# Performance work log

Measured on AMD Instinct MI355X. Metric: run time of the kernel, lower is better.

The kernel has to match this reference:

```python
import jax, jax.numpy as jnp
import numpy as np

B, T, N, D, H, NMASK = 8192, 2, 40, 64, 1, 3
EPS = 1e-5


def setup_inputs() -> dict:
    key = jax.random.key(0)
    ks = jax.random.split(key, 12)
    F = T * N * 2 * D  # flattened feature size fed to BatchNorm1d
    return {
        "x": jax.random.normal(ks[0], (B, N, D), jnp.float32),
        "masker": jax.random.uniform(ks[1], (T, NMASK, N, N), jnp.float32, -0.27, 0.27),  # xavier-like
        "ln_gamma": jnp.ones((N,), jnp.float32),
        "ln_beta": jnp.zeros((N,), jnp.float32),
        "gnn_w": jax.random.normal(ks[2], (1, T, H, 2 * D, D), jnp.float32) * 0.05,
        "gnn_b": jax.random.normal(ks[3], (T, H, N, D), jnp.float32) * 0.05,
        "bn_gamma": jnp.ones((H, F), jnp.float32),
        "bn_beta": jnp.zeros((H, F), jnp.float32),
        "bn_mean": jax.random.normal(ks[4], (H, F), jnp.float32) * 0.1,
        "bn_var": jax.random.uniform(ks[5], (H, F), jnp.float32, 0.5, 1.5),
        "gate_w": jax.random.normal(ks[6], (N * D, N), jnp.float32) * 0.02,
        "gate_b": jnp.zeros((N,), jnp.float32),
    }


def reference(x, masker, ln_gamma, ln_beta, gnn_w, gnn_b, bn_gamma, bn_beta, bn_mean, bn_var, gate_w, gate_b):
    b = x.shape[0]
    # broadcast input to towers: (B, T, N, D)
    h = jnp.broadcast_to(x[:, None], (b, T, N, D))
    # adjacency from product of mask matrices: (T, N, N)
    adj = jax.nn.relu(jnp.prod(masker, axis=1))
    mask = (adj != 0).astype(x.dtype)
    # LayerNorm(num_fields) applied on transposed adj == normalize over rows (axis -2)
    mu = adj.mean(axis=-2, keepdims=True)
    var = adj.var(axis=-2, keepdims=True)
    ln = (adj - mu) / jnp.sqrt(var + EPS) * ln_gamma[:, None] + ln_beta[:, None]
    x_masked = ln + (1.0 - mask) * (-1e9) + jnp.eye(N, dtype=x.dtype)
    # softmax over rows (dim=1 of (T,N,N)) then re-mask
    A = jax.nn.softmax(x_masked, axis=1) * mask  # (T, N, N)
    for idx in range(H):
        # nei[b,t,n,d] = sum_m h[b,t,m,d] * A[t,m,n]
        nei = jnp.einsum('btmd,tmn->btnd', h, A)
        hc = jnp.concatenate([h, nei], axis=-1)  # (B,T,N,2D)
        flat = hc.reshape(b, -1)
        flat = (flat - bn_mean[idx]) / jnp.sqrt(bn_var[idx] + EPS) * bn_gamma[idx] + bn_beta[idx]
        hc = flat.reshape(b, T, N, 2 * D)
        # per-tower transform: (B,T,N,2D) x (T,2D,D) -> (B,T,N,D)
        h = jnp.einsum('btnf,tfd->btnd', hc, gnn_w[0, :, idx]) + gnn_b[:, idx]
    # attention pooling over fields
    logits = h.reshape(b, T, N * D) @ gate_w + gate_b  # (B,T,N)
    w = jax.nn.softmax(logits, axis=2)
    return jnp.sum(h * w[..., None], axis=2)  # (B, T, D)
```

## Files before the change

### kernel.cpp

```cpp
#include <hip/hip_runtime.h>
#include <hip/hip_bf16.h>
#include <stdint.h>

typedef float v4f __attribute__((ext_vector_type(4)));
typedef short v8s __attribute__((ext_vector_type(8)));

#define NB 40

__device__ __forceinline__ unsigned short f2b(float f) {
  __hip_bfloat16 h = __float2bfloat16(f);
  unsigned short u;
  __builtin_memcpy(&u, &h, 2);
  return u;
}
__device__ __forceinline__ unsigned pk2(float lo, float hi) {
  __hip_bfloat162 h = __float22bfloat162_rn(make_float2(lo, hi));
  unsigned u;
  __builtin_memcpy(&u, &h, 4);
  return u;
}
__device__ __forceinline__ float b2f16(unsigned short h) {
  return __uint_as_float(((unsigned)h) << 16);
}
__device__ __forceinline__ float blo(unsigned u) { return __uint_as_float(u << 16); }
__device__ __forceinline__ float bhi(unsigned u) { return __uint_as_float(u & 0xFFFF0000u); }


__global__ __launch_bounds__(256) void prep(
    const float* __restrict__ x, const float* __restrict__ masker,
    const float* __restrict__ ln_gamma, const float* __restrict__ ln_beta,
    const float* __restrict__ gnn_w, const float* __restrict__ gnn_b,
    const float* __restrict__ bn_gamma, const float* __restrict__ bn_beta,
    const float* __restrict__ bn_mean, const float* __restrict__ bn_var,
    const float* __restrict__ gate_w,
    unsigned short* __restrict__ A1pk, unsigned short* __restrict__ W2pk,
    unsigned short* __restrict__ Gpk, float* __restrict__ s1,
    float* __restrict__ sNT, float* __restrict__ bias2T,
    unsigned short* __restrict__ xk, unsigned short* __restrict__ xb16)
{
  __shared__ float AtL[2 * NB * NB];
  const int tid = threadIdx.x;

  {
    const int lane = tid & 63, bq = tid >> 6;
    const int b = blockIdx.x * 4 + bq;
    const float* xb = x + (size_t)b * 2560 + lane;
    unsigned u[20];
    #pragma unroll
    for (int mp = 0; mp < 20; ++mp)
      u[mp] = pk2(xb[(2*mp)*64], xb[(2*mp+1)*64]);
    unsigned short* dst = xk + ((size_t)b * 64 + lane) * 40;
    #pragma unroll
    for (int i = 0; i < 5; ++i)
      *(uint4*)(dst + i*8) = make_uint4(u[4*i], u[4*i+1], u[4*i+2], u[4*i+3]);
    const float4* xs4 = (const float4*)(x + (size_t)blockIdx.x * 10240);
    uint2* xd2 = (uint2*)(xb16 + (size_t)blockIdx.x * 10240);
    #pragma unroll
    for (int it = 0; it < 10; ++it) {
      float4 v = xs4[it*256 + tid];
      xd2[it*256 + tid] = make_uint2(pk2(v.x, v.y), pk2(v.z, v.w));
    }
  }

  if (blockIdx.x < 40) {
    const int gid = blockIdx.x * 256 + tid, gsz = 40 * 256;
    for (int e = gid; e < 16384; e += gsz) {
      int frag = e >> 9, rem = e & 511, lane = rem >> 3, jj = rem & 7;
      int t = frag >> 4, ks = (frag >> 2) & 3, dt = frag & 3;
      int f = ks*32 + (lane >> 4)*8 + jj, d = dt*16 + (lane & 15);
      W2pk[e] = f2b(gnn_w[t*8192 + f*64 + d]);
    }
    for (int e = gid; e < 122880; e += gsz) {
      int frag = e >> 9, rem = e & 511, lane = rem >> 3, jj = rem & 7;
      int kt = frag / 3, jt = frag % 3;
      int fl = kt*32 + (lane >> 4)*8 + jj, j = jt*16 + (lane & 15);
      Gpk[e] = f2b(j < NB ? gate_w[fl*NB + j] : 0.f);
    }
    for (int e = gid; e < 5120; e += gsz) {
      int t = e / 2560, n = (e % 2560) / 64, d = e & 63;
      int F = (t*NB + n)*128 + d;
      s1[e] = bn_gamma[F] * rsqrtf(bn_var[F] + 1e-5f);
    }
    for (int e = gid; e < 5120; e += gsz) {
      int t = e / 2560, d = (e % 2560) / 40, n = e % 40;
      int F = (t*NB + n)*128 + 64 + d;
      sNT[e] = bn_gamma[F] * rsqrtf(bn_var[F] + 1e-5f);
    }
    for (int e = gid; e < 5120; e += gsz) {
      int t = e / 2560, d = (e % 2560) / 40, n = e % 40;
      float acc = gnn_b[(t*NB + n)*64 + d];
      int Fb = (t*NB + n)*128;
      for (int f = 0; f < 128; ++f) {
        float s = bn_gamma[Fb+f] * rsqrtf(bn_var[Fb+f] + 1e-5f);
        float o = bn_beta[Fb+f] - bn_mean[Fb+f] * s;
        acc += o * gnn_w[t*8192 + f*64 + d];
      }
      bias2T[e] = acc;
    }
  } else if (blockIdx.x == 40) {
    for (int col = tid; col < 2 * NB; col += 256) {
      int t = col / NB, n = col % NB;
      float adj[NB];
      for (int m = 0; m < NB; ++m) {
        float p = masker[((t*3+0)*NB+m)*NB+n]
                * masker[((t*3+1)*NB+m)*NB+n]
                * masker[((t*3+2)*NB+m)*NB+n];
        adj[m] = p > 0.f ? p : 0.f;
      }
      float mu = 0.f;
      for (int m = 0; m < NB; ++m) mu += adj[m];
      mu *= (1.f/NB);
      float var = 0.f;
      for (int m = 0; m < NB; ++m) { float dv = adj[m]-mu; var += dv*dv; }
      var *= (1.f/NB);
      float inv = rsqrtf(var + 1e-5f);
      float xm[NB]; float mx = -3e38f;
      for (int m = 0; m < NB; ++m) {
        float lnv = (adj[m]-mu)*inv*ln_gamma[m] + ln_beta[m];
        float v = lnv + (adj[m] != 0.f ? 0.f : -1e9f) + (m==n ? 1.f : 0.f);
        xm[m] = v; mx = fmaxf(mx, v);
      }
      float ssum = 0.f;
      for (int m = 0; m < NB; ++m) { xm[m] = __expf(xm[m]-mx); ssum += xm[m]; }
      float isum = 1.f/ssum;
      for (int m = 0; m < NB; ++m)
        AtL[(t*NB+n)*NB+m] = (adj[m] != 0.f) ? xm[m]*isum : 0.f;
    }
    __syncthreads();
    for (int e = tid; e < 6144; e += 256) {
      int frag = e >> 9, rem = e & 511, lane = rem >> 3, jj = rem & 7;
      int t = frag / 6, r2 = frag % 6, nt = r2 >> 1, ks = r2 & 1;
      int n = nt*16 + (lane & 15);
      int m = ks*32 + (lane >> 4)*8 + jj;
      A1pk[e] = f2b((n < NB && m < NB) ? AtL[(t*NB+n)*NB+m] : 0.f);
    }
  }
}

__global__ __launch_bounds__(256) void kernelM(
    const unsigned short* __restrict__ xb16, const unsigned short* __restrict__ xk,
    const unsigned short* __restrict__ A1pk, const unsigned short* __restrict__ W2pk,
    const unsigned short* __restrict__ Gpk, const float* __restrict__ s1,
    const float* __restrict__ sNT, const float* __restrict__ bias2T,
    const float* __restrict__ gate_b, float* __restrict__ out)
{
  __shared__ __align__(16) unsigned short hc[160 * 136];
  __shared__ __align__(16) unsigned short hL[4 * 2568];
  __shared__ float pj[16 * 48];
  __shared__ float wgt[4 * NB];

  const int tid = threadIdx.x;
  const int lane = tid & 63;
  const int w = tid >> 6;
  const int l = lane & 15, q = lane >> 4;
  const int b0 = blockIdx.x * 4;
  unsigned* hcU = (unsigned*)hc;

  v8s b1[4][2];
  #pragma unroll
  for (int i = 0; i < 4; ++i)
    #pragma unroll
    for (int ks = 0; ks < 2; ++ks)
      b1[i][ks] = *(const v8s*)(xk + ((size_t)b0*64 + (w*4+i)*16 + l)*40 + ks*32 + q*8);
  v8s a1[2][3][2];
  #pragma unroll
  for (int t = 0; t < 2; ++t)
    #pragma unroll
    for (int nt = 0; nt < 3; ++nt)
      #pragma unroll
      for (int ks = 0; ks < 2; ++ks)
        a1[t][nt][ks] = *(const v8s*)(A1pk + (((t*3+nt)*2+ks) << 9) + lane*8);
  v8s w2[2][4];
  #pragma unroll
  for (int t = 0; t < 2; ++t)
    #pragma unroll
    for (int ks = 0; ks < 4; ++ks)
      w2[t][ks] = *(const v8s*)(W2pk + (((t*4+ks)*4 + w) << 9) + lane*8);

  uint4 xr[5];

  #pragma unroll
  for (int t = 0; t < 2; ++t) {
    #pragma unroll
    for (int it = 0; it < 5; ++it) {
      const int c = it*256 + tid;
      const int row = c >> 3, dp8 = c & 7;
      if (t == 0)
        xr[it] = *(const uint4*)((const unsigned*)xb16 + (size_t)b0*1280 + row*32 + dp8*4);
      const uint4 xv = xr[it];
      const int n = row % NB;
      const float4 sA = *(const float4*)(s1 + (t*NB + n)*64 + dp8*8);
      const float4 sB = *(const float4*)(s1 + (t*NB + n)*64 + dp8*8 + 4);
      uint4 p;
      p.x = pk2(blo(xv.x)*sA.x, bhi(xv.x)*sA.y);
      p.y = pk2(blo(xv.y)*sA.z, bhi(xv.y)*sA.w);
      p.z = pk2(blo(xv.z)*sB.x, bhi(xv.z)*sB.y);
      p.w = pk2(blo(xv.w)*sB.z, bhi(xv.w)*sB.w);
      *(uint4*)(hcU + row*68 + dp8*4) = p;
    }
    #pragma unroll
    for (int i = 0; i < 4; ++i) {
      const int R = (w*4+i)*16 + l;
      const int bb = R >> 6, d = R & 63;
      #pragma unroll
      for (int nt = 0; nt < 3; ++nt) {
        v4f acc = {0.f, 0.f, 0.f, 0.f};
        acc = __builtin_amdgcn_mfma_f32_16x16x32_bf16(a1[t][nt][0], b1[i][0], acc, 0, 0, 0);
        acc = __builtin_amdgcn_mfma_f32_16x16x32_bf16(a1[t][nt][1], b1[i][1], acc, 0, 0, 0);
        const float4 sv = *(const float4*)(sNT + (t*64+d)*40 + nt*16 + q*4);
        #pragma unroll
        for (int r = 0; r < 4; ++r) {
          int n = nt*16 + q*4 + r;
          if (n < NB) hc[(bb*NB + n)*136 + 64 + d] = f2b(acc[r]*sv[r]);
        }
      }
    }
    __syncthreads();
    #pragma unroll
    for (int mt = 0; mt < 10; ++mt) {
      v4f acc = {0.f, 0.f, 0.f, 0.f};
      #pragma unroll
      for (int ks = 0; ks < 4; ++ks) {
        v8s af = *(const v8s*)(hc + (mt*16 + l)*136 + ks*32 + q*8);
        acc = __builtin_amdgcn_mfma_f32_16x16x32_bf16(af, w2[t][ks], acc, 0, 0, 0);
      }
      const int d = w*16 + l;
      const int G = mt*16 + q*4;
      const int bb = G / NB, n0 = G - bb*NB;
      const float4 bv = *(const float4*)(bias2T + (t*64+d)*40 + n0);
      #pragma unroll
      for (int r = 0; r < 4; ++r)
        hL[bb*2568 + (n0+r)*64 + d] = f2b(acc[r] + bv[r]);
    }
    __syncthreads();
    v4f ac0 = {0,0,0,0}, ac1 = {0,0,0,0}, ac2 = {0,0,0,0};
    for (int kt = w; kt < 80; kt += 4) {
      v8s bf = *(const v8s*)(hL + (l & 3)*2568 + kt*32 + q*8);
      v8s g0 = *(const v8s*)(Gpk + ((kt*3+0) << 9) + lane*8);
      v8s g1 = *(const v8s*)(Gpk + ((kt*3+1) << 9) + lane*8);
      v8s g2 = *(const v8s*)(Gpk + ((kt*3+2) << 9) + lane*8);
      ac0 = __builtin_amdgcn_mfma_f32_16x16x32_bf16(g0, bf, ac0, 0, 0, 0);
      ac1 = __builtin_amdgcn_mfma_f32_16x16x32_bf16(g1, bf, ac1, 0, 0, 0);
      ac2 = __builtin_amdgcn_mfma_f32_16x16x32_bf16(g2, bf, ac2, 0, 0, 0);
    }
    if (l < 4) {
      #pragma unroll
      for (int r = 0; r < 4; ++r) {
        pj[(w*4 + l)*48 +  0 + q*4 + r] = ac0[r];
        pj[(w*4 + l)*48 + 16 + q*4 + r] = ac1[r];
        pj[(w*4 + l)*48 + 32 + q*4 + r] = ac2[r];
      }
    }
    __syncthreads();
    if (tid < 32) {
      const int bb = tid >> 3, s = tid & 7;
      float lv[5]; float mx = -3e38f;
      #pragma unroll
      for (int i = 0; i < 5; ++i) {
        int j = s*5 + i;
        float v = gate_b[j];
        #pragma unroll
        for (int ww = 0; ww < 4; ++ww) v += pj[(ww*4 + bb)*48 + j];
        lv[i] = v; mx = fmaxf(mx, v);
      }
      #pragma unroll
      for (int m = 1; m < 8; m <<= 1) mx = fmaxf(mx, __shfl_xor(mx, m));
      float es = 0.f;
      #pragma unroll
      for (int i = 0; i < 5; ++i) { lv[i] = __expf(lv[i] - mx); es += lv[i]; }
      #pragma unroll
      for (int m = 1; m < 8; m <<= 1) es += __shfl_xor(es, m);
      float inv = 1.f / es;
      #pragma unroll
      for (int i = 0; i < 5; ++i) wgt[bb*NB + s*5 + i] = lv[i]*inv;
    }
    __syncthreads();
    {
      float accp = 0.f;
      #pragma unroll 8
      for (int n = 0; n < NB; ++n)
        accp += b2f16(hL[w*2568 + n*64 + lane]) * wgt[w*NB + n];
      out[((size_t)(b0 + w)*2 + t)*64 + lane] = accp;
    }
  }
}

extern "C" void kernel_launch(void* const* d_in, const int* in_sizes, int n_in,
                              void* d_out, int out_size, void* d_ws, size_t ws_size,
                              hipStream_t stream) {
  const float* x        = (const float*)d_in[0];
  const float* masker   = (const float*)d_in[1];
  const float* ln_gamma = (const float*)d_in[2];
  const float* ln_beta  = (const float*)d_in[3];
  const float* gnn_w    = (const float*)d_in[4];
  const float* gnn_b    = (const float*)d_in[5];
  const float* bn_gamma = (const float*)d_in[6];
  const float* bn_beta  = (const float*)d_in[7];
  const float* bn_mean  = (const float*)d_in[8];
  const float* bn_var   = (const float*)d_in[9];
  const float* gate_w   = (const float*)d_in[10];
  const float* gate_b   = (const float*)d_in[11];
  float* out = (float*)d_out;

  char* ws = (char*)d_ws;
  unsigned short* A1pk   = (unsigned short*)(ws + 0);
  unsigned short* W2pk   = (unsigned short*)(ws + 12288);
  unsigned short* Gpk    = (unsigned short*)(ws + 45056);
  float*          s1     = (float*)(ws + 290816);
  float*          sNT    = (float*)(ws + 311296);
  float*          bias2T = (float*)(ws + 331904);
  unsigned short* xk     = (unsigned short*)(ws + 352384);
  unsigned short* xb16   = (unsigned short*)(ws + 42295552);

  prep<<<2048, 256, 0, stream>>>(x, masker, ln_gamma, ln_beta, gnn_w, gnn_b,
                                 bn_gamma, bn_beta, bn_mean, bn_var, gate_w,
                                 A1pk, W2pk, Gpk, s1, sNT, bias2T, xk, xb16);
  kernelM<<<2048, 256, 0, stream>>>(xb16, xk, A1pk, W2pk, Gpk,
                                    s1, sNT, bias2T, gate_b, out);
}
```

Before: 265.1 us.

## Fuse fp32-to-bf16 input conversion into main kernel and shrink prep kernel

The prep kernel no longer converts x into two bf16 copies (xk transposed and xb16) in global memory. kernelM now reads fp32 x directly, packs it to bf16 in registers, and builds the transposed operand through shared memory. This removes a full extra write and read pass over the activations, which was the dominant memory traffic. The change also aliases hL onto hc to cut LDS use, sets launch bounds to 3 blocks per CU, loads A and W fragments per tower to reduce register pressure, splits the bias reduction across four lanes, and does the gate softmax with wave shuffles instead of a shared buffer and an extra barrier. The cost is more barriers and an LDS transpose inside the main kernel.

```diff
diff --git a/kernel.cpp b/kernel.cpp
--- a/kernel.cpp
+++ b/kernel.cpp
@@ -27,7 +27,7 @@
 
 
 __global__ __launch_bounds__(256) void prep(
-    const float* __restrict__ x, const float* __restrict__ masker,
+    const float* __restrict__ masker,
     const float* __restrict__ ln_gamma, const float* __restrict__ ln_beta,
     const float* __restrict__ gnn_w, const float* __restrict__ gnn_b,
     const float* __restrict__ bn_gamma, const float* __restrict__ bn_beta,
@@ -35,69 +35,11 @@
     const float* __restrict__ gate_w,
     unsigned short* __restrict__ A1pk, unsigned short* __restrict__ W2pk,
     unsigned short* __restrict__ Gpk, float* __restrict__ s1,
-    float* __restrict__ sNT, float* __restrict__ bias2T,
-    unsigned short* __restrict__ xk, unsigned short* __restrict__ xb16)
+    float* __restrict__ sNT, float* __restrict__ bias2T)
 {
-  __shared__ float AtL[2 * NB * NB];
   const int tid = threadIdx.x;
-
-  {
-    const int lane = tid & 63, bq = tid >> 6;
-    const int b = blockIdx.x * 4 + bq;
-    const float* xb = x + (size_t)b * 2560 + lane;
-    unsigned u[20];
-    #pragma unroll
-    for (int mp = 0; mp < 20; ++mp)
-      u[mp] = pk2(xb[(2*mp)*64], xb[(2*mp+1)*64]);
-    unsigned short* dst = xk + ((size_t)b * 64 + lane) * 40;
-    #pragma unroll
-    for (int i = 0; i < 5; ++i)
-      *(uint4*)(dst + i*8) = make_uint4(u[4*i], u[4*i+1], u[4*i+2], u[4*i+3]);
-    const float4* xs4 = (const float4*)(x + (size_t)blockIdx.x * 10240);
-    uint2* xd2 = (uint2*)(xb16 + (size_t)blockIdx.x * 10240);
-    #pragma unroll
-    for (int it = 0; it < 10; ++it) {
-      float4 v = xs4[it*256 + tid];
-      xd2[it*256 + tid] = make_uint2(pk2(v.x, v.y), pk2(v.z, v.w));
-    }
-  }
-
-  if (blockIdx.x < 40) {
-    const int gid = blockIdx.x * 256 + tid, gsz = 40 * 256;
-    for (int e = gid; e < 16384; e += gsz) {
-      int frag = e >> 9, rem = e & 511, lane = rem >> 3, jj = rem & 7;
-      int t = frag >> 4, ks = (frag >> 2) & 3, dt = frag & 3;
-      int f = ks*32 + (lane >> 4)*8 + jj, d = dt*16 + (lane & 15);
-      W2pk[e] = f2b(gnn_w[t*8192 + f*64 + d]);
-    }
-    for (int e = gid; e < 122880; e += gsz) {
-      int frag = e >> 9, rem = e & 511, lane = rem >> 3, jj = rem & 7;
-      int kt = frag / 3, jt = frag % 3;
-      int fl = kt*32 + (lane >> 4)*8 + jj, j = jt*16 + (lane & 15);
-      Gpk[e] = f2b(j < NB ? gate_w[fl*NB + j] : 0.f);
-    }
-    for (int e = gid; e < 5120; e += gsz) {
-      int t = e / 2560, n = (e % 2560) / 64, d = e & 63;
-      int F = (t*NB + n)*128 + d;
-      s1[e] = bn_gamma[F] * rsqrtf(bn_var[F] + 1e-5f);
-    }
-    for (int e = gid; e < 5120; e += gsz) {
-      int t = e / 2560, d = (e % 2560) / 40, n = e % 40;
-      int F = (t*NB + n)*128 + 64 + d;
-      sNT[e] = bn_gamma[F] * rsqrtf(bn_var[F] + 1e-5f);
-    }
-    for (int e = gid; e < 5120; e += gsz) {
-      int t = e / 2560, d = (e % 2560) / 40, n = e % 40;
-      float acc = gnn_b[(t*NB + n)*64 + d];
-      int Fb = (t*NB + n)*128;
-      for (int f = 0; f < 128; ++f) {
-        float s = bn_gamma[Fb+f] * rsqrtf(bn_var[Fb+f] + 1e-5f);
-        float o = bn_beta[Fb+f] - bn_mean[Fb+f] * s;
-        acc += o * gnn_w[t*8192 + f*64 + d];
-      }
-      bias2T[e] = acc;
-    }
-  } else if (blockIdx.x == 40) {
+  if (blockIdx.x == 0) {
+    __shared__ float AtL[2 * NB * NB];
     for (int col = tid; col < 2 * NB; col += 256) {
       int t = col / NB, n = col % NB;
       float adj[NB];
@@ -134,20 +76,57 @@
       int m = ks*32 + (lane >> 4)*8 + jj;
       A1pk[e] = f2b((n < NB && m < NB) ? AtL[(t*NB+n)*NB+m] : 0.f);
     }
+  } else {
+    const int gid = (blockIdx.x - 1) * 256 + tid, gsz = 63 * 256;
+    for (int e = gid; e < 16384; e += gsz) {
+      int frag = e >> 9, rem = e & 511, lane = rem >> 3, jj = rem & 7;
+      int t = frag >> 4, ks = (frag >> 2) & 3, dt = frag & 3;
+      int f = ks*32 + (lane >> 4)*8 + jj, d = dt*16 + (lane & 15);
+      W2pk[e] = f2b(gnn_w[t*8192 + f*64 + d]);
+    }
+    for (int e = gid; e < 122880; e += gsz) {
+      int frag = e >> 9, rem = e & 511, lane = rem >> 3, jj = rem & 7;
+      int kt = frag / 3, jt = frag % 3;
+      int fl = kt*32 + (lane >> 4)*8 + jj, j = jt*16 + (lane & 15);
+      Gpk[e] = f2b(j < NB ? gate_w[fl*NB + j] : 0.f);
+    }
+    for (int e = gid; e < 5120; e += gsz) {
+      int t = e / 2560, n = (e % 2560) / 64, d = e & 63;
+      int F = (t*NB + n)*128 + d;
+      s1[e] = bn_gamma[F] * rsqrtf(bn_var[F] + 1e-5f);
+    }
+    for (int e = gid; e < 5120; e += gsz) {
+      int t = e / 2560, d = (e % 2560) / 40, n = e % 40;
+      int F = (t*NB + n)*128 + 64 + d;
+      sNT[e] = bn_gamma[F] * rsqrtf(bn_var[F] + 1e-5f);
+    }
+    for (int e4 = gid; e4 < 20480; e4 += gsz) {
+      int e = e4 >> 2, part = e4 & 3;
+      int t = e / 2560, d = (e % 2560) / 40, n = e % 40;
+      float acc = (part == 0) ? gnn_b[(t*NB + n)*64 + d] : 0.f;
+      int Fb = (t*NB + n)*128;
+      int f0 = part * 32;
+      for (int f = f0; f < f0 + 32; ++f) {
+        float s = bn_gamma[Fb+f] * rsqrtf(bn_var[Fb+f] + 1e-5f);
+        float o = bn_beta[Fb+f] - bn_mean[Fb+f] * s;
+        acc += o * gnn_w[t*8192 + f*64 + d];
+      }
+      acc += __shfl_xor(acc, 1);
+      acc += __shfl_xor(acc, 2);
+      if (part == 0) bias2T[e] = acc;
+    }
   }
 }
 
-__global__ __launch_bounds__(256) void kernelM(
-    const unsigned short* __restrict__ xb16, const unsigned short* __restrict__ xk,
+__global__ __launch_bounds__(256, 3) void kernelM(
+    const float* __restrict__ x,
     const unsigned short* __restrict__ A1pk, const unsigned short* __restrict__ W2pk,
     const unsigned short* __restrict__ Gpk, const float* __restrict__ s1,
     const float* __restrict__ sNT, const float* __restrict__ bias2T,
     const float* __restrict__ gate_b, float* __restrict__ out)
 {
   __shared__ __align__(16) unsigned short hc[160 * 136];
-  __shared__ __align__(16) unsigned short hL[4 * 2568];
   __shared__ float pj[16 * 48];
-  __shared__ float wgt[4 * NB];
 
   const int tid = threadIdx.x;
   const int lane = tid & 63;
@@ -155,38 +134,61 @@
   const int l = lane & 15, q = lane >> 4;
   const int b0 = blockIdx.x * 4;
   unsigned* hcU = (unsigned*)hc;
-
+  unsigned short* hL = hc;
+
+  uint4 xr[5];
+  #pragma unroll
+  for (int it = 0; it < 5; ++it) {
+    const int c = it * 256 + tid, row = c >> 3, dp8 = c & 7;
+    const float* xp = x + (size_t)b0 * 2560 + row * 64 + dp8 * 8;
+    const float4 f0 = *(const float4*)xp;
+    const float4 f1 = *(const float4*)(xp + 4);
+    xr[it] = make_uint4(pk2(f0.x, f0.y), pk2(f0.z, f0.w),
+                        pk2(f1.x, f1.y), pk2(f1.z, f1.w));
+  }
+  if (tid < 12) hcU[5120 + tid] = 0u;
+  #pragma unroll
+  for (int it = 0; it < 5; ++it) {
+    const int c = it * 256 + tid, row = c >> 3, dp8 = c & 7;
+    const int bq = row / NB, n = row - bq * NB;
+    unsigned short* base = hc + (bq * 64 + dp8 * 8) * NB + n;
+    const unsigned uu0 = xr[it].x, uu1 = xr[it].y, uu2 = xr[it].z, uu3 = xr[it].w;
+    base[0*NB] = (unsigned short)(uu0 & 0xFFFF);
+    base[1*NB] = (unsigned short)(uu0 >> 16);
+    base[2*NB] = (unsigned short)(uu1 & 0xFFFF);
+    base[3*NB] = (unsigned short)(uu1 >> 16);
+    base[4*NB] = (unsigned short)(uu2 & 0xFFFF);
+    base[5*NB] = (unsigned short)(uu2 >> 16);
+    base[6*NB] = (unsigned short)(uu3 & 0xFFFF);
+    base[7*NB] = (unsigned short)(uu3 >> 16);
+  }
+  __syncthreads();
   v8s b1[4][2];
   #pragma unroll
   for (int i = 0; i < 4; ++i)
     #pragma unroll
     for (int ks = 0; ks < 2; ++ks)
-      b1[i][ks] = *(const v8s*)(xk + ((size_t)b0*64 + (w*4+i)*16 + l)*40 + ks*32 + q*8);
-  v8s a1[2][3][2];
-  #pragma unroll
-  for (int t = 0; t < 2; ++t)
-    #pragma unroll
-    for (int nt = 0; nt < 3; ++nt)
-      #pragma unroll
-      for (int ks = 0; ks < 2; ++ks)
-        a1[t][nt][ks] = *(const v8s*)(A1pk + (((t*3+nt)*2+ks) << 9) + lane*8);
-  v8s w2[2][4];
-  #pragma unroll
-  for (int t = 0; t < 2; ++t)
-    #pragma unroll
-    for (int ks = 0; ks < 4; ++ks)
-      w2[t][ks] = *(const v8s*)(W2pk + (((t*4+ks)*4 + w) << 9) + lane*8);
-
-  uint4 xr[5];
+      b1[i][ks] = *(const v8s*)(hc + ((w * 4 + i) * 16 + l) * NB + ks * 32 + q * 8);
+  __syncthreads();
 
   #pragma unroll
   for (int t = 0; t < 2; ++t) {
+    if (t) __syncthreads();
+
+    v8s a1[3][2], w2[4];
+    #pragma unroll
+    for (int nt = 0; nt < 3; ++nt)
+      #pragma unroll
+      for (int ks = 0; ks < 2; ++ks)
+        a1[nt][ks] = *(const v8s*)(A1pk + (((t*3 + nt)*2 + ks) << 9) + lane*8);
+    #pragma unroll
+    for (int ks = 0; ks < 4; ++ks)
+      w2[ks] = *(const v8s*)(W2pk + (((t*4 + ks)*4 + w) << 9) + lane*8);
+
     #pragma unroll
     for (int it = 0; it < 5; ++it) {
       const int c = it*256 + tid;
       const int row = c >> 3, dp8 = c & 7;
-      if (t == 0)
-        xr[it] = *(const uint4*)((const unsigned*)xb16 + (size_t)b0*1280 + row*32 + dp8*4);
       const uint4 xv = xr[it];
       const int n = row % NB;
       const float4 sA = *(const float4*)(s1 + (t*NB + n)*64 + dp8*8);
@@ -205,8 +207,8 @@
       #pragma unroll
       for (int nt = 0; nt < 3; ++nt) {
         v4f acc = {0.f, 0.f, 0.f, 0.f};
-        acc = __builtin_amdgcn_mfma_f32_16x16x32_bf16(a1[t][nt][0], b1[i][0], acc, 0, 0, 0);
-        acc = __builtin_amdgcn_mfma_f32_16x16x32_bf16(a1[t][nt][1], b1[i][1], acc, 0, 0, 0);
+        acc = __builtin_amdgcn_mfma_f32_16x16x32_bf16(a1[nt][0], b1[i][0], acc, 0, 0, 0);
+        acc = __builtin_amdgcn_mfma_f32_16x16x32_bf16(a1[nt][1], b1[i][1], acc, 0, 0, 0);
         const float4 sv = *(const float4*)(sNT + (t*64+d)*40 + nt*16 + q*4);
         #pragma unroll
         for (int r = 0; r < 4; ++r) {
@@ -216,21 +218,32 @@
       }
     }
     __syncthreads();
+    unsigned pkr0[10], pkr1[10];
     #pragma unroll
     for (int mt = 0; mt < 10; ++mt) {
       v4f acc = {0.f, 0.f, 0.f, 0.f};
       #pragma unroll
       for (int ks = 0; ks < 4; ++ks) {
         v8s af = *(const v8s*)(hc + (mt*16 + l)*136 + ks*32 + q*8);
-        acc = __builtin_amdgcn_mfma_f32_16x16x32_bf16(af, w2[t][ks], acc, 0, 0, 0);
+        acc = __builtin_amdgcn_mfma_f32_16x16x32_bf16(af, w2[ks], acc, 0, 0, 0);
       }
       const int d = w*16 + l;
       const int G = mt*16 + q*4;
       const int bb = G / NB, n0 = G - bb*NB;
       const float4 bv = *(const float4*)(bias2T + (t*64+d)*40 + n0);
-      #pragma unroll
-      for (int r = 0; r < 4; ++r)
-        hL[bb*2568 + (n0+r)*64 + d] = f2b(acc[r] + bv[r]);
+      pkr0[mt] = pk2(acc[0] + bv.x, acc[1] + bv.y);
+      pkr1[mt] = pk2(acc[2] + bv.z, acc[3] + bv.w);
+    }
+    __syncthreads();
+    #pragma unroll
+    for (int mt = 0; mt < 10; ++mt) {
+      const int d = w*16 + l;
+      const int G = mt*16 + q*4;
+      const int bb = G / NB, n0 = G - bb*NB;
+      hL[bb*2568 + (n0+0)*64 + d] = (unsigned short)(pkr0[mt] & 0xFFFF);
+      hL[bb*2568 + (n0+1)*64 + d] = (unsigned short)(pkr0[mt] >> 16);
+      hL[bb*2568 + (n0+2)*64 + d] = (unsigned short)(pkr1[mt] & 0xFFFF);
+      hL[bb*2568 + (n0+3)*64 + d] = (unsigned short)(pkr1[mt] >> 16);
     }
     __syncthreads();
     v4f ac0 = {0,0,0,0}, ac1 = {0,0,0,0}, ac2 = {0,0,0,0};
@@ -252,34 +265,25 @@
       }
     }
     __syncthreads();
-    if (tid < 32) {
-      const int bb = tid >> 3, s = tid & 7;
-      float lv[5]; float mx = -3e38f;
-      #pragma unroll
-      for (int i = 0; i < 5; ++i) {
-        int j = s*5 + i;
-        float v = gate_b[j];
+    {
+      float v = -3.0e38f;
+      if (lane < NB) {
+        v = gate_b[lane];
         #pragma unroll
-        for (int ww = 0; ww < 4; ++ww) v += pj[(ww*4 + bb)*48 + j];
-        lv[i] = v; mx = fmaxf(mx, v);
-      }
-      #pragma unroll
-      for (int m = 1; m < 8; m <<= 1) mx = fmaxf(mx, __shfl_xor(mx, m));
-      float es = 0.f;
-      #pragma unroll
-      for (int i = 0; i < 5; ++i) { lv[i] = __expf(lv[i] - mx); es += lv[i]; }
-      #pragma unroll
-      for (int m = 1; m < 8; m <<= 1) es += __shfl_xor(es, m);
-      float inv = 1.f / es;
-      #pragma unroll
-      for (int i = 0; i < 5; ++i) wgt[bb*NB + s*5 + i] = lv[i]*inv;
-    }
-    __syncthreads();
-    {
+        for (int ww = 0; ww < 4; ++ww) v += pj[(ww*4 + w)*48 + lane];
+      }
+      float mx = v;
+      #pragma unroll
+      for (int m = 1; m < 64; m <<= 1) mx = fmaxf(mx, __shfl_xor(mx, m));
+      float e = (lane < NB) ? __expf(v - mx) : 0.f;
+      float es = e;
+      #pragma unroll
+      for (int m = 1; m < 64; m <<= 1) es += __shfl_xor(es, m);
+      const float wgt = e / es;
       float accp = 0.f;
-      #pragma unroll 8
+      #pragma unroll
       for (int n = 0; n < NB; ++n)
-        accp += b2f16(hL[w*2568 + n*64 + lane]) * wgt[w*NB + n];
+        accp += b2f16(hL[w*2568 + n*64 + lane]) * __shfl(wgt, n);
       out[((size_t)(b0 + w)*2 + t)*64 + lane] = accp;
     }
   }
@@ -309,12 +313,10 @@
   float*          s1     = (float*)(ws + 290816);
   float*          sNT    = (float*)(ws + 311296);
   float*          bias2T = (float*)(ws + 331904);
-  unsigned short* xk     = (unsigned short*)(ws + 352384);
-  unsigned short* xb16   = (unsigned short*)(ws + 42295552);
-
-  prep<<<2048, 256, 0, stream>>>(x, masker, ln_gamma, ln_beta, gnn_w, gnn_b,
-                                 bn_gamma, bn_beta, bn_mean, bn_var, gate_w,
-                                 A1pk, W2pk, Gpk, s1, sNT, bias2T, xk, xb16);
-  kernelM<<<2048, 256, 0, stream>>>(xb16, xk, A1pk, W2pk, Gpk,
+
+  prep<<<64, 256, 0, stream>>>(masker, ln_gamma, ln_beta, gnn_w, gnn_b,
+                               bn_gamma, bn_beta, bn_mean, bn_var, gate_w,
+                               A1pk, W2pk, Gpk, s1, sNT, bias2T);
+  kernelM<<<2048, 256, 0, stream>>>(x, A1pk, W2pk, Gpk,
                                     s1, sNT, bias2T, gate_b, out);
 }
```

Result: slower. 276.8 us (+4.4%).
